# Kernel tuning notes

Hardware: AMD Instinct MI355X
Metric: run time of the kernel (lower is better)

The kernel has to match this reference:

```python
import jax, jax.numpy as jnp
import numpy as np

N = 10000        # nodes
E = 320000       # edges (before self-loops)
F_IN = 128       # num_feature
H1, C1 = 16, 16  # GAT1: heads=16, out=16 -> concat 256
D = 256          # GAT2: heads=1, out=256
G = 64           # graphs in batch
L = 10           # num_label
NEG_SLOPE = 0.2


def setup_inputs() -> dict:
    key = jax.random.key(0)
    ks = jax.random.split(key, 13)
    sc = lambda f: 1.0 / np.sqrt(f)
    inp = {
        "x": jax.random.normal(ks[0], (N, F_IN), jnp.float32),
        "edge_index": jax.random.randint(ks[1], (2, E), 0, N, dtype=jnp.int32),
        "batch": jnp.sort(jax.random.randint(ks[2], (N,), 0, G, dtype=jnp.int32)),
        "W1": jax.random.normal(ks[3], (F_IN, H1 * C1), jnp.float32) * sc(F_IN),
        "a_src1": jax.random.normal(ks[4], (H1, C1), jnp.float32) * sc(C1),
        "a_dst1": jax.random.normal(ks[5], (H1, C1), jnp.float32) * sc(C1),
        "b1": jnp.zeros((H1 * C1,), jnp.float32),
        "W2": jax.random.normal(ks[6], (H1 * C1, D), jnp.float32) * sc(H1 * C1),
        "a_src2": jax.random.normal(ks[7], (1, D), jnp.float32) * sc(D),
        "a_dst2": jax.random.normal(ks[8], (1, D), jnp.float32) * sc(D),
        "b2": jnp.zeros((D,), jnp.float32),
        "lin_w": jax.random.normal(ks[9], (D, L), jnp.float32) * sc(D),
        "lin_b": jnp.zeros((L,), jnp.float32),
    }
    return inp


def _leaky(v):
    return jnp.where(v >= 0, v, NEG_SLOPE * v)


def gat_conv(x, src, dst, W, a_src, a_dst, bias, heads, ch):
    """PyG GATConv (eval mode): gather, leaky-relu logits, segment softmax over dst, scatter-add."""
    n = x.shape[0]
    h = (x @ W).reshape(n, heads, ch)                       # [N,H,C]
    al_s = jnp.sum(h * a_src, axis=-1)                      # [N,H]
    al_d = jnp.sum(h * a_dst, axis=-1)                      # [N,H]
    e = _leaky(al_s[src] + al_d[dst])                       # [Etot,H]
    m = jax.ops.segment_max(e, dst, num_segments=n)         # [N,H]
    m = jnp.where(jnp.isfinite(m), m, 0.0)
    ex = jnp.exp(e - m[dst])
    s = jax.ops.segment_sum(ex, dst, num_segments=n)        # [N,H] (>0: self-loops)
    alpha = ex / s[dst]                                     # [Etot,H]
    out = jax.ops.segment_sum(alpha[:, :, None] * h[src], dst, num_segments=n)
    return out.reshape(n, heads * ch) + bias


def reference(x, edge_index, batch, W1, a_src1, a_dst1, b1, W2, a_src2, a_dst2, b2, lin_w, lin_b):
    n = x.shape[0]
    loops = jnp.arange(n, dtype=edge_index.dtype)
    src = jnp.concatenate([edge_index[0], loops])           # add_self_loops=True (PyG default)
    dst = jnp.concatenate([edge_index[1], loops])

    h = gat_conv(x, src, dst, W1, a_src1, a_dst1, b1, H1, C1)
    h = jax.nn.relu(h)
    h = gat_conv(h, src, dst, W2, a_src2, a_dst2, b2, 1, D)

    # global_mean_pool over graph ids
    sums = jax.ops.segment_sum(h, batch, num_segments=G)    # [G,D]
    cnts = jax.ops.segment_sum(jnp.ones((n,), h.dtype), batch, num_segments=G)
    pooled = sums / jnp.maximum(cnts, 1.0)[:, None]

    # dropout is identity in eval mode
    return pooled @ lin_w + lin_b                           # [G,L]
```

## Files before the change

kernel.cpp:

```cpp
#include <hip/hip_runtime.h>
#include <hip/hip_bf16.h>
#include <math.h>

#define NEG_SLOPE 0.2f
#define LDS_FENCE() asm volatile("s_waitcnt lgkmcnt(0)" ::: "memory")

#define CSR_NB 128

template <int K, bool L1HEADS>
__device__ __forceinline__ void gemm_body(int bx,
    const float* __restrict__ X, const float* __restrict__ W,
    float* __restrict__ C, const float* __restrict__ a_src,
    const float* __restrict__ a_dst, float* __restrict__ als,
    float* __restrict__ ald, int N) {
    int t = threadIdx.x;
    int lane = t & 63, wave = t >> 6;
    int n0 = bx * 16 + wave * 4;
    if (n0 >= N) return;
    const float* Wp = W + lane * 4;
    const float* Xr[4];
#pragma unroll
    for (int rr = 0; rr < 4; ++rr) {
        int r = min(n0 + rr, N - 1);
        Xr[rr] = X + (size_t)__builtin_amdgcn_readfirstlane(r) * K;
    }
    float4 acc[4] = {};
#pragma unroll 2
    for (int k = 0; k < K; k += 4) {
        float4 w0 = *(const float4*)(Wp + (size_t)k * 256);
        float4 w1 = *(const float4*)(Wp + (size_t)(k + 1) * 256);
        float4 w2 = *(const float4*)(Wp + (size_t)(k + 2) * 256);
        float4 w3 = *(const float4*)(Wp + (size_t)(k + 3) * 256);
#pragma unroll
        for (int rr = 0; rr < 4; ++rr) {
            float4 xv = *(const float4*)(Xr[rr] + k);
            acc[rr].x = fmaf(xv.x, w0.x, acc[rr].x);
            acc[rr].y = fmaf(xv.x, w0.y, acc[rr].y);
            acc[rr].z = fmaf(xv.x, w0.z, acc[rr].z);
            acc[rr].w = fmaf(xv.x, w0.w, acc[rr].w);
            acc[rr].x = fmaf(xv.y, w1.x, acc[rr].x);
            acc[rr].y = fmaf(xv.y, w1.y, acc[rr].y);
            acc[rr].z = fmaf(xv.y, w1.z, acc[rr].z);
            acc[rr].w = fmaf(xv.y, w1.w, acc[rr].w);
            acc[rr].x = fmaf(xv.z, w2.x, acc[rr].x);
            acc[rr].y = fmaf(xv.z, w2.y, acc[rr].y);
            acc[rr].z = fmaf(xv.z, w2.z, acc[rr].z);
            acc[rr].w = fmaf(xv.z, w2.w, acc[rr].w);
            acc[rr].x = fmaf(xv.w, w3.x, acc[rr].x);
            acc[rr].y = fmaf(xv.w, w3.y, acc[rr].y);
            acc[rr].z = fmaf(xv.w, w3.z, acc[rr].z);
            acc[rr].w = fmaf(xv.w, w3.w, acc[rr].w);
        }
    }
    float4 asv = *(const float4*)(a_src + lane * 4);
    float4 adv = *(const float4*)(a_dst + lane * 4);
#pragma unroll
    for (int rr = 0; rr < 4; ++rr) {
        int n = n0 + rr;
        if (n >= N) break;
        *(float4*)(C + (size_t)n * 256 + lane * 4) = acc[rr];
        float s = acc[rr].x * asv.x + acc[rr].y * asv.y + acc[rr].z * asv.z + acc[rr].w * asv.w;
        float d = acc[rr].x * adv.x + acc[rr].y * adv.y + acc[rr].z * adv.z + acc[rr].w * adv.w;
        if (L1HEADS) {
            s += __shfl_xor(s, 1); s += __shfl_xor(s, 2);
            d += __shfl_xor(d, 1); d += __shfl_xor(d, 2);
            if ((lane & 3) == 0) {
                als[n * 16 + (lane >> 2)] = s;
                ald[n * 16 + (lane >> 2)] = d;
            }
        } else {
#pragma unroll
            for (int off = 1; off <= 32; off <<= 1) {
                s += __shfl_xor(s, off);
                d += __shfl_xor(d, off);
            }
            if (lane == 0) { als[n] = s; ald[n] = d; }
        }
    }
}

__global__ __launch_bounds__(256) void k_hist_gemm1(
    const int* __restrict__ ei, int E, int N, int NP, int CE, int* __restrict__ hist,
    const float* __restrict__ X, const float* __restrict__ W1, float* __restrict__ A,
    const float* __restrict__ as1, const float* __restrict__ ad1,
    float* __restrict__ als1, float* __restrict__ ald1) {
    if (blockIdx.x < CSR_NB) {
        __shared__ int lhist[384];
        int t = threadIdx.x, b = blockIdx.x;
        for (int p = t; p < 384; p += 256) lhist[p] = 0;
        __syncthreads();
        int Etot = E + N;
        int e0 = b * CE, e1 = min(Etot, e0 + CE);
        for (int e = e0 + t; e < e1; e += 256) {
            int d = (e < E) ? ei[E + e] : (e - E);
            atomicAdd(&lhist[d >> 5], 1);
        }
        __syncthreads();
        for (int p = t; p < NP; p += 256) hist[b * NP + p] = lhist[p];
    } else {
        gemm_body<128, true>(blockIdx.x - CSR_NB, X, W1, A, as1, ad1, als1, ald1, N);
    }
}

__global__ __launch_bounds__(256) void k_gemm2(
    const float* __restrict__ X, const float* __restrict__ W, float* __restrict__ C,
    const float* __restrict__ as2, const float* __restrict__ ad2,
    float* __restrict__ als, float* __restrict__ ald, int N) {
    gemm_body<256, false>(blockIdx.x, X, W, C, as2, ad2, als, ald, N);
}

__global__ __launch_bounds__(512) void k_partscan(int* __restrict__ hist, int NP,
                                                  int* __restrict__ partBase,
                                                  int* __restrict__ rowptr, int N) {
    __shared__ int wsums[8];
    int t = threadIdx.x, lane = t & 63, wave = t >> 6;
    int tot = 0;
    if (t < NP)
        for (int b = 0; b < CSR_NB; ++b) tot += hist[b * NP + t];
    int x = tot;
#pragma unroll
    for (int off = 1; off < 64; off <<= 1) {
        int v = __shfl_up(x, off);
        if (lane >= off) x += v;
    }
    if (lane == 63) wsums[wave] = x;
    __syncthreads();
    int wp = 0;
    for (int w = 0; w < 8; ++w) {
        int s = wsums[w];
        if (w < wave) wp += s;
    }
    int excl = wp + x - tot;
    if (t < NP) {
        partBase[t] = excl;
        int run = excl;
        for (int b = 0; b < CSR_NB; ++b) {
            int h = hist[b * NP + t];
            hist[b * NP + t] = run;
            run += h;
        }
        if (t == NP - 1) {
            partBase[NP] = run;
            rowptr[N] = run;
        }
    }
}

__global__ __launch_bounds__(256) void k_partscatter(const int* __restrict__ ei, int E, int N,
                                                     int NP, int CE,
                                                     const int* __restrict__ hist,
                                                     int* __restrict__ tmp) {
    __shared__ int cursor[384];
    int t = threadIdx.x, b = blockIdx.x;
    for (int p = t; p < NP; p += 256) cursor[p] = hist[b * NP + p];
    __syncthreads();
    int Etot = E + N;
    int e0 = b * CE, e1 = min(Etot, e0 + CE);
    for (int e = e0 + t; e < e1; e += 256) {
        int s, d;
        if (e < E) { s = ei[e]; d = ei[E + e]; } else { s = d = e - E; }
        int pos = atomicAdd(&cursor[d >> 5], 1);
        tmp[pos] = (s << 5) | (d & 31);
    }
}

__global__ __launch_bounds__(256) void k_csr_final(const int* __restrict__ tmp,
                                                   const int* __restrict__ partBase,
                                                   int* __restrict__ rowptr,
                                                   int* __restrict__ col, int N) {
    __shared__ int dcnt[32], dcur[32];
    int t = threadIdx.x, p = blockIdx.x;
    int base = partBase[p], end = partBase[p + 1];
    if (t < 32) dcnt[t] = 0;
    __syncthreads();
    for (int i = base + t; i < end; i += 256) atomicAdd(&dcnt[tmp[i] & 31], 1);
    __syncthreads();
    if (t < 32) {
        int v = dcnt[t];
        int x = v;
#pragma unroll
        for (int off = 1; off < 32; off <<= 1) {
            int u = __shfl_up(x, off);
            if (t >= off) x += u;
        }
        int excl = x - v;
        dcur[t] = excl;
        int dst = (p << 5) + t;
        if (dst < N) rowptr[dst] = base + excl;
    }
    __syncthreads();
    for (int i = base + t; i < end; i += 256) {
        int v = tmp[i];
        int pos = atomicAdd(&dcur[v & 31], 1);
        col[base + pos] = v >> 5;
    }
}

__global__ __launch_bounds__(256) void k_gather_h1(
    const int* __restrict__ rowptr, const int* __restrict__ col,
    const float* __restrict__ H, const float* __restrict__ als,
    const float* __restrict__ ald, const float* __restrict__ bias,
    float* __restrict__ out, int N) {
    __shared__ float2 sw[4][64];
    int wave = threadIdx.x >> 6, lane = threadIdx.x & 63;
    int n = blockIdx.x * 4 + wave;
    if (n >= N) return;
    int hf = blockIdx.y;
    int coff = hf * 128 + lane * 2;
    int start = rowptr[n], end = rowptr[n + 1];
    float aldv = ald[n];
    float2 acc = {0.f, 0.f};
    float swsum = 0.f;
    const float* Hh = H + coff;
    for (int base = start; base < end; base += 64) {
        int len = min(64, end - base);
        int s = 0;
        float w = 0.f;
        if (lane < len) {
            s = col[base + lane];
            float v = als[s] + aldv;
            v = v >= 0.f ? v : NEG_SLOPE * v;
            w = __expf(v);
        }
        swsum += w;
        sw[wave][lane] = make_float2(__int_as_float(s), w);
        LDS_FENCE();
#pragma unroll 4
        for (int e = 0; e < len; ++e) {
            float2 p = sw[wave][e];
            int se = __float_as_int(p.x);
            float we = p.y;
            float2 hv = *(const float2*)(Hh + (size_t)se * 256);
            acc.x = fmaf(we, hv.x, acc.x);
            acc.y = fmaf(we, hv.y, acc.y);
        }
        LDS_FENCE();
    }
#pragma unroll
    for (int off = 32; off >= 1; off >>= 1) swsum += __shfl_xor(swsum, off);
    float inv = 1.0f / swsum;
    float2 b2v = *(const float2*)(bias + coff);
    float2 r;
    r.x = fmaf(acc.x, inv, b2v.x);
    r.y = fmaf(acc.y, inv, b2v.y);
    *(float2*)(out + (size_t)n * 256 + coff) = r;
}

__global__ __launch_bounds__(256) void k_gather_h16(
    const int* __restrict__ rowptr, const int* __restrict__ col,
    const float* __restrict__ H, const float* __restrict__ als,
    const float* __restrict__ ald, const float* __restrict__ bias,
    float* __restrict__ out, int N) {
    __shared__ int s_lds[4][64];
    __shared__ float w_lds[4][64 * 8];
    int wave = threadIdx.x >> 6, lane = threadIdx.x & 63;
    int n = blockIdx.x * 4 + wave;
    if (n >= N) return;
    int hf = blockIdx.y;
    int coff = hf * 128 + lane * 2;
    int start = rowptr[n], end = rowptr[n + 1];
    int hW = (hf << 3) + (lane & 7);
    int eW = lane >> 3;
    float aldW = ald[n * 16 + hW];
    float2 acc = {0.f, 0.f};
    float swp = 0.f;
    const float* Hh = H + coff;
    for (int base = start; base < end; base += 64) {
        int len = min(64, end - base);
        if (lane < len) s_lds[wave][lane] = col[base + lane];
        LDS_FENCE();
#pragma unroll
        for (int k = 0; k < 8; ++k) {
            int esub = (k << 3) + eW;
            float w = 0.f;
            if (esub < len) {
                int s = s_lds[wave][esub];
                float v = als[s * 16 + hW] + aldW;
                v = v >= 0.f ? v : NEG_SLOPE * v;
                w = __expf(v);
            }
            w_lds[wave][(esub << 3) + (lane & 7)] = w;
            swp += w;
        }
        LDS_FENCE();
#pragma unroll 4
        for (int e = 0; e < len; ++e) {
            int se = s_lds[wave][e];
            float we = w_lds[wave][(e << 3) + (lane >> 3)];
            float2 hv = *(const float2*)(Hh + (size_t)se * 256);
            acc.x = fmaf(we, hv.x, acc.x);
            acc.y = fmaf(we, hv.y, acc.y);
        }
        LDS_FENCE();
    }
    swp += __shfl_xor(swp, 8);
    swp += __shfl_xor(swp, 16);
    swp += __shfl_xor(swp, 32);
    float inv = 1.0f / __shfl(swp, lane >> 3);
    float2 b2v = *(const float2*)(bias + coff);
    float2 r;
    r.x = fmaxf(fmaf(acc.x, inv, b2v.x), 0.f);
    r.y = fmaxf(fmaf(acc.y, inv, b2v.y), 0.f);
    *(float2*)(out + (size_t)n * 256 + coff) = r;
}

__device__ __forceinline__ int lower_bound_i(const int* __restrict__ a, int n, int v) {
    int lo = 0, hi = n;
    while (lo < hi) {
        int mid = (lo + hi) >> 1;
        if (a[mid] < v) lo = mid + 1; else hi = mid;
    }
    return lo;
}

__global__ __launch_bounds__(1024) void k_pool_final(const float* __restrict__ B,
                                                     const int* __restrict__ batch,
                                                     const float* __restrict__ lw,
                                                     const float* __restrict__ lb,
                                                     float* __restrict__ out,
                                                     int N, int L) {
    __shared__ float psum[4][256];
    __shared__ float csum[256];
    int t = threadIdx.x;
    int c = t & 255, q = t >> 8;
    int g = blockIdx.x;
    int lo = lower_bound_i(batch, N, g);
    int hi = lower_bound_i(batch, N, g + 1);
    int len = hi - lo;
    int per = (len + 3) >> 2;
    int s0 = lo + q * per, s1 = min(hi, s0 + per);
    float acc = 0.f;
    for (int r = s0; r < s1; ++r) acc += B[(size_t)r * 256 + c];
    psum[q][c] = acc;
    __syncthreads();
    if (t < 256) csum[t] = psum[0][t] + psum[1][t] + psum[2][t] + psum[3][t];
    __syncthreads();
    int wave = t >> 6, lane = t & 63;
    if (wave < L) {
        int l = wave;
        float a = csum[lane] * lw[lane * L + l] +
                  csum[lane + 64] * lw[(lane + 64) * L + l] +
                  csum[lane + 128] * lw[(lane + 128) * L + l] +
                  csum[lane + 192] * lw[(lane + 192) * L + l];
#pragma unroll
        for (int off = 32; off >= 1; off >>= 1) a += __shfl_xor(a, off);
        if (lane == 0) out[g * L + l] = a / fmaxf((float)len, 1.0f) + lb[l];
    }
}

extern "C" void kernel_launch(void* const* d_in, const int* in_sizes, int n_in,
                              void* d_out, int out_size, void* d_ws, size_t ws_size,
                              hipStream_t stream) {
    const float* x   = (const float*)d_in[0];
    const int*   ei  = (const int*)d_in[1];
    const int*   bat = (const int*)d_in[2];
    const float* W1  = (const float*)d_in[3];
    const float* as1 = (const float*)d_in[4];
    const float* ad1 = (const float*)d_in[5];
    const float* b1  = (const float*)d_in[6];
    const float* W2  = (const float*)d_in[7];
    const float* as2 = (const float*)d_in[8];
    const float* ad2 = (const float*)d_in[9];
    const float* b2  = (const float*)d_in[10];
    const float* lw  = (const float*)d_in[11];
    const float* lb  = (const float*)d_in[12];
    float* out = (float*)d_out;

    const int N = in_sizes[2];
    const int E = in_sizes[1] / 2;
    const int G = 64, L = 10;
    const int Etot = E + N;
    const int NP = (N + 31) >> 5;
    const int CE = (Etot + CSR_NB - 1) / CSR_NB;

    float* A    = (float*)d_ws;
    float* B    = A + (size_t)N * 256;
    float* als1 = B + (size_t)N * 256;
    float* ald1 = als1 + (size_t)N * 16;
    float* als2 = ald1 + (size_t)N * 16;
    float* ald2 = als2 + N;
    int* rowptr   = (int*)(ald2 + N);
    int* col      = rowptr + N + 1;
    int* tmp      = col + Etot;
    int* hist     = tmp + Etot;
    int* partBase = hist + CSR_NB * NP;

    const int BS = 256;
    auto nb = [](int n, int b) { return (n + b - 1) / b; };
    int nodes4 = nb(N, 4);
    int rows16 = nb(N, 16);

    k_hist_gemm1<<<CSR_NB + rows16, BS, 0, stream>>>(ei, E, N, NP, CE, hist,
                                                     x, W1, A, as1, ad1, als1, ald1);
    k_partscan<<<1, 512, 0, stream>>>(hist, NP, partBase, rowptr, N);
    k_partscatter<<<CSR_NB, BS, 0, stream>>>(ei, E, N, NP, CE, hist, tmp);
    k_csr_final<<<NP, BS, 0, stream>>>(tmp, partBase, rowptr, col, N);

    k_gather_h16<<<dim3(nodes4, 2), BS, 0, stream>>>(rowptr, col, A, als1, ald1, b1, B, N);

    k_gemm2<<<rows16, BS, 0, stream>>>(B, W2, A, as2, ad2, als2, ald2, N);
    k_gather_h1<<<dim3(nodes4, 2), BS, 0, stream>>>(rowptr, col, A, als2, ald2, b2, B, N);

    k_pool_final<<<G, 1024, 0, stream>>>(B, bat, lw, lb, out, N, L);
}
```

Baseline: 234.8 us.

## Fuse CSR build into bucketed scatter and widen gathers to float4 per node

Replaces the histogram, partition-scan and partition-scatter pipeline with fixed-capacity buckets per 32-node partition. A global atomic counter hands out slots, so two kernel launches and a serial scan disappear, and rowptr becomes per-node start/end pairs. The gather kernels now cover all 256 channels with float4 loads in a single block per node rather than two half-width blocks. That removes the duplicated edge-weight and index work. The risk is that any partition with more than CSR_CAP edges silently loses edges, and the workspace grows to NP*CAP entries.

Measured after the change: 236.6 us. No clear change (+0.8%).

```diff
diff --git a/kernel.cpp b/kernel.cpp
--- a/kernel.cpp
+++ b/kernel.cpp
@@ -6,6 +6,7 @@
 #define LDS_FENCE() asm volatile("s_waitcnt lgkmcnt(0)" ::: "memory")
 
 #define CSR_NB 128
+#define CSR_CAP 2048
 
 template <int K, bool L1HEADS>
 __device__ __forceinline__ void gemm_body(int bx,
@@ -79,8 +80,9 @@
     }
 }
 
-__global__ __launch_bounds__(256) void k_hist_gemm1(
-    const int* __restrict__ ei, int E, int N, int NP, int CE, int* __restrict__ hist,
+__global__ __launch_bounds__(256) void k_scatter_gemm1(
+    const int* __restrict__ ei, int E, int N, int NP, int CE,
+    int* __restrict__ gcount, int* __restrict__ tmp,
     const float* __restrict__ X, const float* __restrict__ W1, float* __restrict__ A,
     const float* __restrict__ as1, const float* __restrict__ ad1,
     float* __restrict__ als1, float* __restrict__ ald1) {
@@ -96,7 +98,18 @@
             atomicAdd(&lhist[d >> 5], 1);
         }
         __syncthreads();
-        for (int p = t; p < NP; p += 256) hist[b * NP + p] = lhist[p];
+        for (int p = t; p < NP; p += 256) {
+            int c = lhist[p];
+            lhist[p] = c ? atomicAdd(&gcount[p], c) : 0;
+        }
+        __syncthreads();
+        for (int e = e0 + t; e < e1; e += 256) {
+            int s, d;
+            if (e < E) { s = ei[e]; d = ei[E + e]; } else { s = d = e - E; }
+            int p = d >> 5;
+            int pos = atomicAdd(&lhist[p], 1);
+            tmp[p * CSR_CAP + min(pos, CSR_CAP - 1)] = (s << 5) | (d & 31);
+        }
     } else {
         gemm_body<128, true>(blockIdx.x - CSR_NB, X, W1, A, as1, ad1, als1, ald1, N);
     }
@@ -109,71 +122,17 @@
     gemm_body<256, false>(blockIdx.x, X, W, C, as2, ad2, als, ald, N);
 }
 
-__global__ __launch_bounds__(512) void k_partscan(int* __restrict__ hist, int NP,
-                                                  int* __restrict__ partBase,
-                                                  int* __restrict__ rowptr, int N) {
-    __shared__ int wsums[8];
-    int t = threadIdx.x, lane = t & 63, wave = t >> 6;
-    int tot = 0;
-    if (t < NP)
-        for (int b = 0; b < CSR_NB; ++b) tot += hist[b * NP + t];
-    int x = tot;
-#pragma unroll
-    for (int off = 1; off < 64; off <<= 1) {
-        int v = __shfl_up(x, off);
-        if (lane >= off) x += v;
-    }
-    if (lane == 63) wsums[wave] = x;
-    __syncthreads();
-    int wp = 0;
-    for (int w = 0; w < 8; ++w) {
-        int s = wsums[w];
-        if (w < wave) wp += s;
-    }
-    int excl = wp + x - tot;
-    if (t < NP) {
-        partBase[t] = excl;
-        int run = excl;
-        for (int b = 0; b < CSR_NB; ++b) {
-            int h = hist[b * NP + t];
-            hist[b * NP + t] = run;
-            run += h;
-        }
-        if (t == NP - 1) {
-            partBase[NP] = run;
-            rowptr[N] = run;
-        }
-    }
-}
-
-__global__ __launch_bounds__(256) void k_partscatter(const int* __restrict__ ei, int E, int N,
-                                                     int NP, int CE,
-                                                     const int* __restrict__ hist,
-                                                     int* __restrict__ tmp) {
-    __shared__ int cursor[384];
-    int t = threadIdx.x, b = blockIdx.x;
-    for (int p = t; p < NP; p += 256) cursor[p] = hist[b * NP + p];
-    __syncthreads();
-    int Etot = E + N;
-    int e0 = b * CE, e1 = min(Etot, e0 + CE);
-    for (int e = e0 + t; e < e1; e += 256) {
-        int s, d;
-        if (e < E) { s = ei[e]; d = ei[E + e]; } else { s = d = e - E; }
-        int pos = atomicAdd(&cursor[d >> 5], 1);
-        tmp[pos] = (s << 5) | (d & 31);
-    }
-}
-
 __global__ __launch_bounds__(256) void k_csr_final(const int* __restrict__ tmp,
-                                                   const int* __restrict__ partBase,
-                                                   int* __restrict__ rowptr,
+                                                   const int* __restrict__ gcount,
+                                                   int2* __restrict__ rowse,
                                                    int* __restrict__ col, int N) {
     __shared__ int dcnt[32], dcur[32];
     int t = threadIdx.x, p = blockIdx.x;
-    int base = partBase[p], end = partBase[p + 1];
+    int base = p * CSR_CAP;
+    int cnt = min(gcount[p], CSR_CAP);
     if (t < 32) dcnt[t] = 0;
     __syncthreads();
-    for (int i = base + t; i < end; i += 256) atomicAdd(&dcnt[tmp[i] & 31], 1);
+    for (int i = t; i < cnt; i += 256) atomicAdd(&dcnt[tmp[base + i] & 31], 1);
     __syncthreads();
     if (t < 32) {
         int v = dcnt[t];
@@ -186,18 +145,18 @@
         int excl = x - v;
         dcur[t] = excl;
         int dst = (p << 5) + t;
-        if (dst < N) rowptr[dst] = base + excl;
-    }
-    __syncthreads();
-    for (int i = base + t; i < end; i += 256) {
-        int v = tmp[i];
+        if (dst < N) rowse[dst] = make_int2(base + excl, base + excl + v);
+    }
+    __syncthreads();
+    for (int i = t; i < cnt; i += 256) {
+        int v = tmp[base + i];
         int pos = atomicAdd(&dcur[v & 31], 1);
         col[base + pos] = v >> 5;
     }
 }
 
 __global__ __launch_bounds__(256) void k_gather_h1(
-    const int* __restrict__ rowptr, const int* __restrict__ col,
+    const int2* __restrict__ rowse, const int* __restrict__ col,
     const float* __restrict__ H, const float* __restrict__ als,
     const float* __restrict__ ald, const float* __restrict__ bias,
     float* __restrict__ out, int N) {
@@ -205,13 +164,12 @@
     int wave = threadIdx.x >> 6, lane = threadIdx.x & 63;
     int n = blockIdx.x * 4 + wave;
     if (n >= N) return;
-    int hf = blockIdx.y;
-    int coff = hf * 128 + lane * 2;
-    int start = rowptr[n], end = rowptr[n + 1];
+    int2 se = rowse[n];
+    int start = se.x, end = se.y;
     float aldv = ald[n];
-    float2 acc = {0.f, 0.f};
+    float4 acc = {0.f, 0.f, 0.f, 0.f};
     float swsum = 0.f;
-    const float* Hh = H + coff;
+    const float* Hh = H + lane * 4;
     for (int base = start; base < end; base += 64) {
         int len = min(64, end - base);
         int s = 0;
@@ -228,80 +186,85 @@
 #pragma unroll 4
         for (int e = 0; e < len; ++e) {
             float2 p = sw[wave][e];
-            int se = __float_as_int(p.x);
+            int s2 = __float_as_int(p.x);
             float we = p.y;
-            float2 hv = *(const float2*)(Hh + (size_t)se * 256);
+            float4 hv = *(const float4*)(Hh + (size_t)s2 * 256);
             acc.x = fmaf(we, hv.x, acc.x);
             acc.y = fmaf(we, hv.y, acc.y);
+            acc.z = fmaf(we, hv.z, acc.z);
+            acc.w = fmaf(we, hv.w, acc.w);
         }
         LDS_FENCE();
     }
 #pragma unroll
     for (int off = 32; off >= 1; off >>= 1) swsum += __shfl_xor(swsum, off);
     float inv = 1.0f / swsum;
-    float2 b2v = *(const float2*)(bias + coff);
-    float2 r;
-    r.x = fmaf(acc.x, inv, b2v.x);
-    r.y = fmaf(acc.y, inv, b2v.y);
-    *(float2*)(out + (size_t)n * 256 + coff) = r;
+    float4 bv = *(const float4*)(bias + lane * 4);
+    float4 r;
+    r.x = fmaf(acc.x, inv, bv.x);
+    r.y = fmaf(acc.y, inv, bv.y);
+    r.z = fmaf(acc.z, inv, bv.z);
+    r.w = fmaf(acc.w, inv, bv.w);
+    *(float4*)(out + (size_t)n * 256 + lane * 4) = r;
 }
 
 __global__ __launch_bounds__(256) void k_gather_h16(
-    const int* __restrict__ rowptr, const int* __restrict__ col,
+    const int2* __restrict__ rowse, const int* __restrict__ col,
     const float* __restrict__ H, const float* __restrict__ als,
     const float* __restrict__ ald, const float* __restrict__ bias,
     float* __restrict__ out, int N) {
     __shared__ int s_lds[4][64];
-    __shared__ float w_lds[4][64 * 8];
+    __shared__ float w_lds[4][64 * 16];
     int wave = threadIdx.x >> 6, lane = threadIdx.x & 63;
     int n = blockIdx.x * 4 + wave;
     if (n >= N) return;
-    int hf = blockIdx.y;
-    int coff = hf * 128 + lane * 2;
-    int start = rowptr[n], end = rowptr[n + 1];
-    int hW = (hf << 3) + (lane & 7);
-    int eW = lane >> 3;
-    float aldW = ald[n * 16 + hW];
-    float2 acc = {0.f, 0.f};
+    int2 se = rowse[n];
+    int start = se.x, end = se.y;
+    int hq = lane & 15;
+    int eq = lane >> 4;
+    float aldW = ald[n * 16 + hq];
+    float4 acc = {0.f, 0.f, 0.f, 0.f};
     float swp = 0.f;
-    const float* Hh = H + coff;
+    const float* Hh = H + lane * 4;
     for (int base = start; base < end; base += 64) {
         int len = min(64, end - base);
         if (lane < len) s_lds[wave][lane] = col[base + lane];
         LDS_FENCE();
 #pragma unroll
-        for (int k = 0; k < 8; ++k) {
-            int esub = (k << 3) + eW;
-            float w = 0.f;
+        for (int k = 0; k < 16; ++k) {
+            int esub = (k << 2) + eq;
             if (esub < len) {
                 int s = s_lds[wave][esub];
-                float v = als[s * 16 + hW] + aldW;
+                float v = als[s * 16 + hq] + aldW;
                 v = v >= 0.f ? v : NEG_SLOPE * v;
-                w = __expf(v);
+                float w = __expf(v);
+                w_lds[wave][(esub << 4) + hq] = w;
+                swp += w;
             }
-            w_lds[wave][(esub << 3) + (lane & 7)] = w;
-            swp += w;
         }
         LDS_FENCE();
 #pragma unroll 4
         for (int e = 0; e < len; ++e) {
-            int se = s_lds[wave][e];
-            float we = w_lds[wave][(e << 3) + (lane >> 3)];
-            float2 hv = *(const float2*)(Hh + (size_t)se * 256);
+            int s2 = s_lds[wave][e];
+            float we = w_lds[wave][(e << 4) + (lane >> 2)];
+            float4 hv = *(const float4*)(Hh + (size_t)s2 * 256);
             acc.x = fmaf(we, hv.x, acc.x);
             acc.y = fmaf(we, hv.y, acc.y);
-        }
-        LDS_FENCE();
-    }
-    swp += __shfl_xor(swp, 8);
+            acc.z = fmaf(we, hv.z, acc.z);
+            acc.w = fmaf(we, hv.w, acc.w);
+        }
+        LDS_FENCE();
+    }
     swp += __shfl_xor(swp, 16);
     swp += __shfl_xor(swp, 32);
-    float inv = 1.0f / __shfl(swp, lane >> 3);
-    float2 b2v = *(const float2*)(bias + coff);
-    float2 r;
-    r.x = fmaxf(fmaf(acc.x, inv, b2v.x), 0.f);
-    r.y = fmaxf(fmaf(acc.y, inv, b2v.y), 0.f);
-    *(float2*)(out + (size_t)n * 256 + coff) = r;
+    float inv = 1.0f / __shfl(swp, lane >> 2);
+    float4 bv = *(const float4*)(bias + lane * 4);
+    float4 r;
+    r.x = fmaxf(fmaf(acc.x, inv, bv.x), 0.f);
+    r.y = fmaxf(fmaf(acc.y, inv, bv.y), 0.f);
+    r.z = fmaxf(fmaf(acc.z, inv, bv.z), 0.f);
+    r.w = fmaxf(fmaf(acc.w, inv, bv.w), 0.f);
+    *(float4*)(out + (size_t)n * 256 + lane * 4) = r;
 }
 
 __device__ __forceinline__ int lower_bound_i(const int* __restrict__ a, int n, int v) {
@@ -379,27 +342,25 @@
     float* ald1 = als1 + (size_t)N * 16;
     float* als2 = ald1 + (size_t)N * 16;
     float* ald2 = als2 + N;
-    int* rowptr   = (int*)(ald2 + N);
-    int* col      = rowptr + N + 1;
-    int* tmp      = col + Etot;
-    int* hist     = tmp + Etot;
-    int* partBase = hist + CSR_NB * NP;
+    int2* rowse = (int2*)(ald2 + N);
+    int* col    = (int*)(rowse + N);
+    int* tmp    = col + (size_t)NP * CSR_CAP;
+    int* gcount = tmp + (size_t)NP * CSR_CAP;
 
     const int BS = 256;
     auto nb = [](int n, int b) { return (n + b - 1) / b; };
     int nodes4 = nb(N, 4);
     int rows16 = nb(N, 16);
 
-    k_hist_gemm1<<<CSR_NB + rows16, BS, 0, stream>>>(ei, E, N, NP, CE, hist,
-                                                     x, W1, A, as1, ad1, als1, ald1);
-    k_partscan<<<1, 512, 0, stream>>>(hist, NP, partBase, rowptr, N);
-    k_partscatter<<<CSR_NB, BS, 0, stream>>>(ei, E, N, NP, CE, hist, tmp);
-    k_csr_final<<<NP, BS, 0, stream>>>(tmp, partBase, rowptr, col, N);
-
-    k_gather_h16<<<dim3(nodes4, 2), BS, 0, stream>>>(rowptr, col, A, als1, ald1, b1, B, N);
+    hipMemsetAsync(gcount, 0, NP * sizeof(int), stream);
+    k_scatter_gemm1<<<CSR_NB + rows16, BS, 0, stream>>>(ei, E, N, NP, CE, gcount, tmp,
+                                                        x, W1, A, as1, ad1, als1, ald1);
+    k_csr_final<<<NP, BS, 0, stream>>>(tmp, gcount, rowse, col, N);
+
+    k_gather_h16<<<nodes4, BS, 0, stream>>>(rowse, col, A, als1, ald1, b1, B, N);
 
     k_gemm2<<<rows16, BS, 0, stream>>>(B, W2, A, as2, ad2, als2, ald2, N);
-    k_gather_h1<<<dim3(nodes4, 2), BS, 0, stream>>>(rowptr, col, A, als2, ald2, b2, B, N);
+    k_gather_h1<<<nodes4, BS, 0, stream>>>(rowse, col, A, als2, ald2, b2, B, N);
 
     k_pool_final<<<G, 1024, 0, stream>>>(B, bat, lw, lb, out, N, L);
 }
```
